# Performance work log

Hardware: AMD Instinct MI355X
Metric: run time of the kernel (lower is better)

The kernel has to match this reference:

```python
import jax, jax.numpy as jnp
import numpy as np

DIM = 1024
NUM_HEADS = 16
HEAD_DIM = DIM // NUM_HEADS
SCALE = HEAD_DIM ** (-0.5)


def setup_inputs() -> dict:
    key = jax.random.key(0)
    ks = jax.random.split(key, 10)
    b, nq, nkv = 1, 4096, 4096
    s = DIM ** -0.5
    return {
        "q": jax.random.normal(ks[0], (b, nq, DIM), jnp.float32),
        "kv": jax.random.normal(ks[1], (b, nkv, DIM), jnp.float32),
        "q_w": jax.random.normal(ks[2], (DIM, DIM), jnp.float32) * s,
        "q_b": jnp.zeros((DIM,), jnp.float32),
        "k_w": jax.random.normal(ks[3], (DIM, DIM), jnp.float32) * s,
        "k_b": jnp.zeros((DIM,), jnp.float32),
        "v_w": jax.random.normal(ks[4], (DIM, DIM), jnp.float32) * s,
        "v_b": jnp.zeros((DIM,), jnp.float32),
        "o_w": jax.random.normal(ks[5], (DIM, DIM), jnp.float32) * s,
        "o_b": jnp.zeros((DIM,), jnp.float32),
    }


def reference(q, kv, q_w, q_b, k_w, k_b, v_w, v_b, o_w, o_b):
    b, nq, _ = q.shape
    nkv = kv.shape[1]
    h, c = NUM_HEADS, HEAD_DIM
    # projections (torch Linear: x @ W^T + b); split into heads
    qh = (q @ q_w.T + q_b).reshape(b, nq, h, c).transpose(0, 2, 1, 3)   # b h nq c
    kh = (kv @ k_w.T + k_b).reshape(b, nkv, h, c).transpose(0, 2, 1, 3)  # b h nkv c
    vh = (kv @ v_w.T + v_b).reshape(b, nkv, h, c).transpose(0, 2, 1, 3)  # b h nkv c
    # full attention score matrix (non-fused, as in source)
    attn = jnp.einsum('bhqc,bhkc->bhqk', qh, kh) * SCALE
    attn = jax.nn.softmax(attn, axis=-1)
    out = jnp.einsum('bhqk,bhkc->bhqc', attn, vh)  # b h nq c
    out = out.transpose(0, 2, 1, 3).reshape(b, nq, h * c)
    out = out @ o_w.T + o_b
    return out
```

## Files before the change

kernel.cpp:

```cpp
#include <hip/hip_runtime.h>


typedef unsigned short ushort_t;
typedef unsigned short ushort4v __attribute__((ext_vector_type(4)));
typedef unsigned short ushort8 __attribute__((ext_vector_type(8)));
typedef __bf16 bf16x8 __attribute__((ext_vector_type(8)));
typedef float f32x4 __attribute__((ext_vector_type(4)));
typedef float f32x16 __attribute__((ext_vector_type(16)));
typedef unsigned int uint4v __attribute__((ext_vector_type(4)));

#define SEQ 4096
#define DIM 1024
#define NH 16
#define HD 64
#define QSCALE 0.18033688011112042f

__device__ inline ushort_t fcvt(float f) {
    return __builtin_bit_cast(ushort_t, (__bf16)f);
}
__device__ inline bf16x8 frag_of(ushort8 t) {
    return __builtin_bit_cast(bf16x8, t);
}
__device__ inline bf16x8 lds_frag(const ushort_t* p) {
    return frag_of(*(const ushort8*)p);
}
__device__ inline unsigned pk2(float a, float b) {
    return (unsigned)fcvt(a) | ((unsigned)fcvt(b) << 16);
}
__device__ inline void plswap(unsigned& a, unsigned& b) {
    asm("v_permlane32_swap_b32 %0, %1" : "+v"(a), "+v"(b));
}
__device__ inline int swz(int row, int col) {
    return row * 64 + (col ^ ((row & 7) << 3));
}
__device__ __attribute__((always_inline)) inline void gload16(
    const ushort_t* g, ushort_t* l)
{
    __builtin_amdgcn_global_load_lds(
        (const __attribute__((address_space(1))) void*)g,
        (__attribute__((address_space(3))) void*)l, 16, 0, 0);
}

__global__ __launch_bounds__(256) void cvt2(
    const float* __restrict__ s0, ushort_t* __restrict__ d0,
    const float* __restrict__ s1, ushort_t* __restrict__ d1, int n8)
{
    const float* s = blockIdx.y ? s1 : s0;
    ushort_t*    d = blockIdx.y ? d1 : d0;
    int i = blockIdx.x * 256 + threadIdx.x;
    if (i >= n8) return;
    const f32x4* sp = (const f32x4*)s + (size_t)i * 2;
    f32x4 a = sp[0], b = sp[1];
    ushort8 o;
    for (int k = 0; k < 4; ++k) { o[k] = fcvt(a[k]); o[k + 4] = fcvt(b[k]); }
    *((ushort8*)d + i) = o;
}

__global__ __launch_bounds__(256) void cvt4(
    const float* __restrict__ s0, ushort_t* __restrict__ d0,
    const float* __restrict__ s1, ushort_t* __restrict__ d1,
    const float* __restrict__ s2, ushort_t* __restrict__ d2,
    const float* __restrict__ s3, ushort_t* __restrict__ d3, int n8)
{
    const float* ss[4] = {s0, s1, s2, s3};
    ushort_t*    dd[4] = {d0, d1, d2, d3};
    const float* s = ss[blockIdx.y];
    ushort_t*    d = dd[blockIdx.y];
    int i = blockIdx.x * 256 + threadIdx.x;
    if (i >= n8) return;
    const f32x4* sp = (const f32x4*)s + (size_t)i * 2;
    f32x4 a = sp[0], b = sp[1];
    ushort8 o;
    for (int k = 0; k < 4; ++k) { o[k] = fcvt(a[k]); o[k + 4] = fcvt(b[k]); }
    *((ushort8*)d + i) = o;
}

template<int BN>
__device__ __attribute__((always_inline)) inline void gemm_core2(
    const ushort_t* __restrict__ A, const ushort_t* __restrict__ W,
    int m0, int n0, int tid, f32x4 (&acc)[4][BN / 32], ushort_t* sLDS)
{
    constexpr int TA = 128 * 64;
    constexpr int TB = BN * 64;
    ushort_t* const aB0 = sLDS;
    ushort_t* const aB1 = sLDS + TA;
    ushort_t* const bB0 = sLDS + 2 * TA;
    ushort_t* const bB1 = sLDS + 2 * TA + TB;

    const int w    = tid >> 6;
    const int lane = tid & 63;
    const int quad = lane >> 4;
    const int l15  = lane & 15;
    const int wm   = w >> 1;
    const int wn   = w & 1;

    const int srow = lane >> 3;
    const int sch  = ((lane & 7) ^ srow) << 3;
    const ushort_t* Ag = A + (size_t)(m0 + w * 32 + srow) * DIM + sch;
    const ushort_t* Bg = W + (size_t)(n0 + w * (BN / 4) + srow) * DIM + sch;
    const int aOff = w * 2048;
    const int bOff = w * (BN * 16);

    for (int i = 0; i < 4; ++i)
        gload16(Ag + (size_t)(i * 8) * DIM, aB0 + aOff + i * 512);
    for (int i = 0; i < BN / 32; ++i)
        gload16(Bg + (size_t)(i * 8) * DIM, bB0 + bOff + i * 512);
    __syncthreads();

    const int cxor = l15 & 7;
    for (int it = 0; it < DIM / 64; ++it) {
        const int cur = it & 1;
        ushort_t* aC = cur ? aB1 : aB0;
        ushort_t* bC = cur ? bB1 : bB0;
        ushort_t* aN = cur ? aB0 : aB1;
        ushort_t* bN = cur ? bB0 : bB1;

        if (it + 1 < DIM / 64) {
            const int k0 = (it + 1) * 64;
            for (int i = 0; i < 4; ++i)
                gload16(Ag + k0 + (size_t)(i * 8) * DIM, aN + aOff + i * 512);
            for (int i = 0; i < BN / 32; ++i)
                gload16(Bg + k0 + (size_t)(i * 8) * DIM, bN + bOff + i * 512);
        }

        for (int kk = 0; kk < 2; ++kk) {
            const int cq = kk * 4 + quad;
            bf16x8 af[4], bf[BN / 32];
            for (int i = 0; i < 4; ++i) {
                int row = wm * 64 + i * 16 + l15;
                af[i] = lds_frag(aC + row * 64 + ((cq ^ cxor) << 3));
            }
            for (int j = 0; j < BN / 32; ++j) {
                int row = wn * (BN / 2) + j * 16 + l15;
                bf[j] = lds_frag(bC + row * 64 + ((cq ^ cxor) << 3));
            }
            for (int i = 0; i < 4; ++i)
                for (int j = 0; j < BN / 32; ++j)
                    acc[i][j] = __builtin_amdgcn_mfma_f32_16x16x32_bf16(
                        af[i], bf[j], acc[i][j], 0, 0, 0);
        }
        __syncthreads();
    }
}

__global__ __launch_bounds__(256, 2) void proj3(
    const ushort_t* __restrict__ Qb, const ushort_t* __restrict__ KVb,
    const ushort_t* __restrict__ qwb, const ushort_t* __restrict__ kwb,
    const ushort_t* __restrict__ vwb,
    const float* __restrict__ q_b, const float* __restrict__ k_b,
    const float* __restrict__ v_b,
    ushort_t* __restrict__ Qp, ushort_t* __restrict__ Kp,
    ushort_t* __restrict__ VpT)
{
    __shared__ __align__(1024) ushort_t sLDS[32768];

    const int z = blockIdx.z;
    const ushort_t* A = z ? KVb : Qb;
    const ushort_t* W = (z == 0) ? qwb : (z == 1 ? kwb : vwb);
    const float* bias = (z == 0) ? q_b : (z == 1 ? k_b : v_b);
    const int tid = threadIdx.x;
    const int m0 = blockIdx.y * 128;
    const int n0 = blockIdx.x * 128;

    f32x4 acc[4][4] = {};
    gemm_core2<128>(A, W, m0, n0, tid, acc, sLDS);

    const int lane = tid & 63, quad = lane >> 4, l15 = lane & 15;
    const int wm = (tid >> 6) >> 1, wn = (tid >> 6) & 1;

    if (z == 2) {
        const int TSTR = 136;
        for (int j = 0; j < 4; ++j) {
            int col = wn * 64 + j * 16 + l15;
            float bj = bias[n0 + col];
            for (int i = 0; i < 4; ++i) {
                int row = wm * 64 + i * 16 + quad * 4;
                ushort4v o4;
                for (int r = 0; r < 4; ++r) o4[r] = fcvt(acc[i][j][r] + bj);
                *(ushort4v*)(sLDS + col * TSTR + row) = o4;
            }
        }
        __syncthreads();
        const int vrow = tid >> 1;
        const int vc   = (tid & 1) * 64;
        ushort_t* dst = VpT + (size_t)(n0 + vrow) * SEQ + m0 + vc;
        const ushort_t* src = sLDS + vrow * TSTR + vc;
        for (int k = 0; k < 8; ++k)
            *(ushort8*)(dst + k * 8) = *(const ushort8*)(src + k * 8);
    } else {
        const float scale = (z == 0) ? QSCALE : 1.0f;
        ushort_t* C = z ? Kp : Qp;
        for (int j = 0; j < 4; ++j) {
            int col = n0 + wn * 64 + j * 16 + l15;
            float bj = bias[col];
            for (int i = 0; i < 4; ++i) {
                int row = m0 + wm * 64 + i * 16 + quad * 4;
                for (int r = 0; r < 4; ++r)
                    C[(size_t)(row + r) * DIM + col] =
                        fcvt((acc[i][j][r] + bj) * scale);
            }
        }
    }
}

__global__ __launch_bounds__(256, 2) void gemm_out(
    const ushort_t* __restrict__ A, const ushort_t* __restrict__ W,
    const float* __restrict__ bias, float* __restrict__ C)
{
    __shared__ __align__(1024) ushort_t sLDS[24576];

    const int tid = threadIdx.x;
    const int m0 = blockIdx.y * 128;
    const int n0 = blockIdx.x * 64;

    f32x4 acc[4][2] = {};
    gemm_core2<64>(A, W, m0, n0, tid, acc, sLDS);

    const int lane = tid & 63, quad = lane >> 4, l15 = lane & 15;
    const int wm = (tid >> 6) >> 1, wn = (tid >> 6) & 1;
    for (int j = 0; j < 2; ++j) {
        int col = n0 + wn * 32 + j * 16 + l15;
        float bj = bias[col];
        for (int i = 0; i < 4; ++i) {
            int row = m0 + wm * 64 + i * 16 + quad * 4;
            for (int r = 0; r < 4; ++r)
                C[(size_t)(row + r) * DIM + col] = acc[i][j][r] + bj;
        }
    }
}

#define TILE 4096
#define BUFE (2 * TILE)
__global__ __launch_bounds__(256, 2) void attn_kernel(
    const ushort_t* __restrict__ Q, const ushort_t* __restrict__ K,
    const ushort_t* __restrict__ VT, ushort_t* __restrict__ O)
{
    __shared__ __align__(16) ushort_t sB[2 * BUFE];

    const int tid  = threadIdx.x;
    const int w    = tid >> 6;
    const int lane = tid & 63;
    const int l31  = lane & 31;
    const int hi   = lane >> 5;
    const int h    = blockIdx.x;
    const int q0   = blockIdx.y * 128 + w * 32;
    const int hHD  = h * HD;

    const int srow0 = tid >> 3;
    const int srow1 = srow0 + 32;
    const int sch   = (tid & 7) << 3;
    const ushort_t* Kg0 = K  + (size_t)srow0 * DIM + hHD + sch;
    const ushort_t* Kg1 = K  + (size_t)srow1 * DIM + hHD + sch;
    const ushort_t* Vg0 = VT + (size_t)(hHD + srow0) * SEQ + sch;
    const ushort_t* Vg1 = VT + (size_t)(hHD + srow1) * SEQ + sch;
    const int lk0 = swz(srow0, sch), lk1 = swz(srow1, sch);

    const ushort_t* qb = Q + (size_t)(q0 + l31) * DIM + hHD + hi * 8;
    bf16x8 qf[4];
    for (int ks = 0; ks < 4; ++ks)
        qf[ks] = frag_of(*(const ushort8*)(qb + ks * 16));

    *(ushort8*)(sB + lk0)        = *(const ushort8*)(Kg0);
    *(ushort8*)(sB + lk1)        = *(const ushort8*)(Kg1);
    *(ushort8*)(sB + TILE + lk0) = *(const ushort8*)(Vg0);
    *(ushort8*)(sB + TILE + lk1) = *(const ushort8*)(Vg1);
    __syncthreads();

    f32x16 oacc[2] = {};
    float l_i = 0.f;

    for (int it = 0; it < SEQ / 64; ++it) {
        const int cur = it & 1;
        const int kvn = (it + 1) * 64;
        ushort_t* bK = sB + cur * BUFE;
        ushort_t* bV = bK + TILE;

        ushort8 gk0, gk1, gv0, gv1;
        if (kvn < SEQ) {
            gk0 = *(const ushort8*)(Kg0 + (size_t)kvn * DIM);
            gk1 = *(const ushort8*)(Kg1 + (size_t)kvn * DIM);
            gv0 = *(const ushort8*)(Vg0 + kvn);
            gv1 = *(const ushort8*)(Vg1 + kvn);
        }

        bf16x8 kf[8], vf[8];
        for (int t = 0; t < 2; ++t)
            for (int ks = 0; ks < 4; ++ks) {
                int r = t * 32 + l31;
                kf[t * 4 + ks] = lds_frag(bK + swz(r, ks * 16 + hi * 8));
            }
        for (int dt = 0; dt < 2; ++dt)
            for (int ks = 0; ks < 4; ++ks) {
                int r = dt * 32 + l31;
                vf[ks * 2 + dt] = lds_frag(bV + swz(r, ks * 16 + hi * 8));
            }

        f32x16 sacc[2] = {};
        for (int t = 0; t < 2; ++t)
            for (int ks = 0; ks < 4; ++ks)
                sacc[t] = __builtin_amdgcn_mfma_f32_32x32x16_bf16(
                    kf[t * 4 + ks], qf[ks], sacc[t], 0, 0, 0);

        float lp = 0.f;
        for (int t = 0; t < 2; ++t)
            for (int r = 0; r < 16; ++r) {
                float p = __builtin_amdgcn_exp2f(sacc[t][r]);
                sacc[t][r] = p;
                lp += p;
            }
        l_i += lp + __shfl_xor(lp, 32);

        for (int ks = 0; ks < 4; ++ks) {
            const int t = ks >> 1, s8 = (ks & 1) * 8;
            unsigned p00 = pk2(sacc[t][s8 + 0], sacc[t][s8 + 1]);
            unsigned p01 = pk2(sacc[t][s8 + 2], sacc[t][s8 + 3]);
            unsigned p10 = pk2(sacc[t][s8 + 4], sacc[t][s8 + 5]);
            unsigned p11 = pk2(sacc[t][s8 + 6], sacc[t][s8 + 7]);
            plswap(p00, p10);
            plswap(p01, p11);
            uint4v wv; wv[0] = p00; wv[1] = p01; wv[2] = p10; wv[3] = p11;
            bf16x8 pf = __builtin_bit_cast(bf16x8, wv);
            for (int dt = 0; dt < 2; ++dt)
                oacc[dt] = __builtin_amdgcn_mfma_f32_32x32x16_bf16(
                    vf[ks * 2 + dt], pf, oacc[dt], 0, 0, 0);
        }

        if (kvn < SEQ) {
            ushort_t* nB = sB + (cur ^ 1) * BUFE;
            *(ushort8*)(nB + lk0)        = gk0;
            *(ushort8*)(nB + lk1)        = gk1;
            *(ushort8*)(nB + TILE + lk0) = gv0;
            *(ushort8*)(nB + TILE + lk1) = gv1;
        }
        __syncthreads();
    }

    float inv = 1.f / l_i;
    int qrow = q0 + l31;
    for (int dt = 0; dt < 2; ++dt)
        for (int g = 0; g < 4; ++g) {
            ushort4v o4;
            for (int r = 0; r < 4; ++r) o4[r] = fcvt(oacc[dt][g * 4 + r] * inv);
            *(ushort4v*)(O + (size_t)qrow * DIM + hHD + dt * 32 + g * 8 + hi * 4) = o4;
        }
}

extern "C" void kernel_launch(void* const* d_in, const int* in_sizes, int n_in,
                              void* d_out, int out_size, void* d_ws, size_t ws_size,
                              hipStream_t stream)
{
    const float* q   = (const float*)d_in[0];
    const float* kv  = (const float*)d_in[1];
    const float* q_w = (const float*)d_in[2];
    const float* q_b = (const float*)d_in[3];
    const float* k_w = (const float*)d_in[4];
    const float* k_b = (const float*)d_in[5];
    const float* v_w = (const float*)d_in[6];
    const float* v_b = (const float*)d_in[7];
    const float* o_w = (const float*)d_in[8];
    const float* o_b = (const float*)d_in[9];
    float* out = (float*)d_out;

    const size_t SD = (size_t)SEQ * DIM;
    const size_t WW = (size_t)DIM * DIM;
    ushort_t* Qp  = (ushort_t*)d_ws;
    ushort_t* Kp  = Qp + SD;
    ushort_t* VpT = Kp + SD;
    ushort_t* AO  = VpT + SD;
    ushort_t* Qb  = AO;
    ushort_t* KVb = AO + SD;
    ushort_t* qwb = KVb + SD;
    ushort_t* kwb = qwb + WW;
    ushort_t* vwb = kwb + WW;
    ushort_t* owb = vwb + WW;

    cvt2<<<dim3((unsigned)(SD / 8 / 256), 2), 256, 0, stream>>>(
        q, Qb, kv, KVb, (int)(SD / 8));
    cvt4<<<dim3((unsigned)(WW / 8 / 256), 4), 256, 0, stream>>>(
        q_w, qwb, k_w, kwb, v_w, vwb, o_w, owb, (int)(WW / 8));

    proj3<<<dim3(DIM / 128, SEQ / 128, 3), 256, 0, stream>>>(
        Qb, KVb, qwb, kwb, vwb, q_b, k_b, v_b, Qp, Kp, VpT);
    attn_kernel<<<dim3(NH, SEQ / 128), 256, 0, stream>>>(Qp, Kp, VpT, AO);
    gemm_out<<<dim3(DIM / 64, SEQ / 128), 256, 0, stream>>>(AO, owb, o_b, out);
}
```

Before: 245.3 us.

## Shrink GEMM K-tile to 32 with new swizzle, smaller out tiles, MFMA row sums

The GEMM core now stages 32-wide K slices instead of 64, using a new LDS swizzle, which cuts shared memory per block so proj3 and gemm_out can run at higher occupancy (launch bounds 3 and 4). gemm_out drops to 64x64 tiles, doubling its grid. In attention, the softmax denominator is accumulated with an extra MFMA against a ones vector instead of scalar adds plus a cross-lane shuffle. The trade-offs are twice as many K iterations and barriers in the GEMMs, and an extra matrix op per attention step.

```diff
diff --git a/kernel.cpp b/kernel.cpp
--- a/kernel.cpp
+++ b/kernel.cpp
@@ -75,13 +75,13 @@
     *((ushort8*)d + i) = o;
 }
 
-template<int BN>
-__device__ __attribute__((always_inline)) inline void gemm_core2(
+template<int BM, int BN>
+__device__ __attribute__((always_inline)) inline void gemm_core3(
     const ushort_t* __restrict__ A, const ushort_t* __restrict__ W,
-    int m0, int n0, int tid, f32x4 (&acc)[4][BN / 32], ushort_t* sLDS)
-{
-    constexpr int TA = 128 * 64;
-    constexpr int TB = BN * 64;
+    int m0, int n0, int tid, f32x4 (&acc)[BM / 32][BN / 32], ushort_t* sLDS)
+{
+    constexpr int TA = BM * 32;
+    constexpr int TB = BN * 32;
     ushort_t* const aB0 = sLDS;
     ushort_t* const aB1 = sLDS + TA;
     ushort_t* const bB0 = sLDS + 2 * TA;
@@ -94,56 +94,53 @@
     const int wm   = w >> 1;
     const int wn   = w & 1;
 
-    const int srow = lane >> 3;
-    const int sch  = ((lane & 7) ^ srow) << 3;
-    const ushort_t* Ag = A + (size_t)(m0 + w * 32 + srow) * DIM + sch;
+    const int srow = lane >> 2;
+    const int sch  = (((lane & 3) ^ ((lane >> 3) & 3)) << 3);
+    const ushort_t* Ag = A + (size_t)(m0 + w * (BM / 4) + srow) * DIM + sch;
     const ushort_t* Bg = W + (size_t)(n0 + w * (BN / 4) + srow) * DIM + sch;
-    const int aOff = w * 2048;
-    const int bOff = w * (BN * 16);
-
-    for (int i = 0; i < 4; ++i)
-        gload16(Ag + (size_t)(i * 8) * DIM, aB0 + aOff + i * 512);
-    for (int i = 0; i < BN / 32; ++i)
-        gload16(Bg + (size_t)(i * 8) * DIM, bB0 + bOff + i * 512);
+    const int aOff = w * (BM / 4) * 32;
+    const int bOff = w * (BN / 4) * 32;
+
+    for (int i = 0; i < BM / 64; ++i)
+        gload16(Ag + (size_t)(i * 16) * DIM, aB0 + aOff + i * 512);
+    for (int i = 0; i < BN / 64; ++i)
+        gload16(Bg + (size_t)(i * 16) * DIM, bB0 + bOff + i * 512);
     __syncthreads();
 
-    const int cxor = l15 & 7;
-    for (int it = 0; it < DIM / 64; ++it) {
+    const int slot = (quad ^ ((l15 >> 1) & 3)) << 3;
+    for (int it = 0; it < DIM / 32; ++it) {
         const int cur = it & 1;
         ushort_t* aC = cur ? aB1 : aB0;
         ushort_t* bC = cur ? bB1 : bB0;
         ushort_t* aN = cur ? aB0 : aB1;
         ushort_t* bN = cur ? bB0 : bB1;
 
-        if (it + 1 < DIM / 64) {
-            const int k0 = (it + 1) * 64;
-            for (int i = 0; i < 4; ++i)
-                gload16(Ag + k0 + (size_t)(i * 8) * DIM, aN + aOff + i * 512);
-            for (int i = 0; i < BN / 32; ++i)
-                gload16(Bg + k0 + (size_t)(i * 8) * DIM, bN + bOff + i * 512);
-        }
-
-        for (int kk = 0; kk < 2; ++kk) {
-            const int cq = kk * 4 + quad;
-            bf16x8 af[4], bf[BN / 32];
-            for (int i = 0; i < 4; ++i) {
-                int row = wm * 64 + i * 16 + l15;
-                af[i] = lds_frag(aC + row * 64 + ((cq ^ cxor) << 3));
-            }
-            for (int j = 0; j < BN / 32; ++j) {
-                int row = wn * (BN / 2) + j * 16 + l15;
-                bf[j] = lds_frag(bC + row * 64 + ((cq ^ cxor) << 3));
-            }
-            for (int i = 0; i < 4; ++i)
-                for (int j = 0; j < BN / 32; ++j)
-                    acc[i][j] = __builtin_amdgcn_mfma_f32_16x16x32_bf16(
-                        af[i], bf[j], acc[i][j], 0, 0, 0);
-        }
+        if (it + 1 < DIM / 32) {
+            const int k0 = (it + 1) * 32;
+            for (int i = 0; i < BM / 64; ++i)
+                gload16(Ag + k0 + (size_t)(i * 16) * DIM, aN + aOff + i * 512);
+            for (int i = 0; i < BN / 64; ++i)
+                gload16(Bg + k0 + (size_t)(i * 16) * DIM, bN + bOff + i * 512);
+        }
+
+        bf16x8 af[BM / 32], bf[BN / 32];
+        for (int i = 0; i < BM / 32; ++i) {
+            int row = wm * (BM / 2) + i * 16 + l15;
+            af[i] = lds_frag(aC + row * 32 + slot);
+        }
+        for (int j = 0; j < BN / 32; ++j) {
+            int row = wn * (BN / 2) + j * 16 + l15;
+            bf[j] = lds_frag(bC + row * 32 + slot);
+        }
+        for (int i = 0; i < BM / 32; ++i)
+            for (int j = 0; j < BN / 32; ++j)
+                acc[i][j] = __builtin_amdgcn_mfma_f32_16x16x32_bf16(
+                    af[i], bf[j], acc[i][j], 0, 0, 0);
         __syncthreads();
     }
 }
 
-__global__ __launch_bounds__(256, 2) void proj3(
+__global__ __launch_bounds__(256, 3) void proj3(
     const ushort_t* __restrict__ Qb, const ushort_t* __restrict__ KVb,
     const ushort_t* __restrict__ qwb, const ushort_t* __restrict__ kwb,
     const ushort_t* __restrict__ vwb,
@@ -152,7 +149,7 @@
     ushort_t* __restrict__ Qp, ushort_t* __restrict__ Kp,
     ushort_t* __restrict__ VpT)
 {
-    __shared__ __align__(1024) ushort_t sLDS[32768];
+    __shared__ __align__(1024) ushort_t sLDS[17536];
 
     const int z = blockIdx.z;
     const ushort_t* A = z ? KVb : Qb;
@@ -163,7 +160,7 @@
     const int n0 = blockIdx.x * 128;
 
     f32x4 acc[4][4] = {};
-    gemm_core2<128>(A, W, m0, n0, tid, acc, sLDS);
+    gemm_core3<128, 128>(A, W, m0, n0, tid, acc, sLDS);
 
     const int lane = tid & 63, quad = lane >> 4, l15 = lane & 15;
     const int wm = (tid >> 6) >> 1, wn = (tid >> 6) & 1;
@@ -203,26 +200,26 @@
     }
 }
 
-__global__ __launch_bounds__(256, 2) void gemm_out(
+__global__ __launch_bounds__(256, 4) void gemm_out(
     const ushort_t* __restrict__ A, const ushort_t* __restrict__ W,
     const float* __restrict__ bias, float* __restrict__ C)
 {
-    __shared__ __align__(1024) ushort_t sLDS[24576];
+    __shared__ __align__(1024) ushort_t sLDS[8192];
 
     const int tid = threadIdx.x;
-    const int m0 = blockIdx.y * 128;
+    const int m0 = blockIdx.y * 64;
     const int n0 = blockIdx.x * 64;
 
-    f32x4 acc[4][2] = {};
-    gemm_core2<64>(A, W, m0, n0, tid, acc, sLDS);
+    f32x4 acc[2][2] = {};
+    gemm_core3<64, 64>(A, W, m0, n0, tid, acc, sLDS);
 
     const int lane = tid & 63, quad = lane >> 4, l15 = lane & 15;
     const int wm = (tid >> 6) >> 1, wn = (tid >> 6) & 1;
     for (int j = 0; j < 2; ++j) {
         int col = n0 + wn * 32 + j * 16 + l15;
         float bj = bias[col];
-        for (int i = 0; i < 4; ++i) {
-            int row = m0 + wm * 64 + i * 16 + quad * 4;
+        for (int i = 0; i < 2; ++i) {
+            int row = m0 + wm * 32 + i * 16 + quad * 4;
             for (int r = 0; r < 4; ++r)
                 C[(size_t)(row + r) * DIM + col] = acc[i][j][r] + bj;
         }
@@ -260,6 +257,9 @@
     for (int ks = 0; ks < 4; ++ks)
         qf[ks] = frag_of(*(const ushort8*)(qb + ks * 16));
 
+    bf16x8 onef;
+    for (int i = 0; i < 8; ++i) onef[i] = (__bf16)1.0f;
+
     *(ushort8*)(sB + lk0)        = *(const ushort8*)(Kg0);
     *(ushort8*)(sB + lk1)        = *(const ushort8*)(Kg1);
     *(ushort8*)(sB + TILE + lk0) = *(const ushort8*)(Vg0);
@@ -267,7 +267,7 @@
     __syncthreads();
 
     f32x16 oacc[2] = {};
-    float l_i = 0.f;
+    f32x16 lacc = {};
 
     for (int it = 0; it < SEQ / 64; ++it) {
         const int cur = it & 1;
@@ -301,14 +301,9 @@
                 sacc[t] = __builtin_amdgcn_mfma_f32_32x32x16_bf16(
                     kf[t * 4 + ks], qf[ks], sacc[t], 0, 0, 0);
 
-        float lp = 0.f;
         for (int t = 0; t < 2; ++t)
-            for (int r = 0; r < 16; ++r) {
-                float p = __builtin_amdgcn_exp2f(sacc[t][r]);
-                sacc[t][r] = p;
-                lp += p;
-            }
-        l_i += lp + __shfl_xor(lp, 32);
+            for (int r = 0; r < 16; ++r)
+                sacc[t][r] = __builtin_amdgcn_exp2f(sacc[t][r]);
 
         for (int ks = 0; ks < 4; ++ks) {
             const int t = ks >> 1, s8 = (ks & 1) * 8;
@@ -323,6 +318,8 @@
             for (int dt = 0; dt < 2; ++dt)
                 oacc[dt] = __builtin_amdgcn_mfma_f32_32x32x16_bf16(
                     vf[ks * 2 + dt], pf, oacc[dt], 0, 0, 0);
+            lacc = __builtin_amdgcn_mfma_f32_32x32x16_bf16(
+                onef, pf, lacc, 0, 0, 0);
         }
 
         if (kvn < SEQ) {
@@ -335,7 +332,7 @@
         __syncthreads();
     }
 
-    float inv = 1.f / l_i;
+    float inv = 1.f / lacc[0];
     int qrow = q0 + l31;
     for (int dt = 0; dt < 2; ++dt)
         for (int g = 0; g < 4; ++g) {
@@ -382,5 +379,5 @@
     proj3<<<dim3(DIM / 128, SEQ / 128, 3), 256, 0, stream>>>(
         Qb, KVb, qwb, kwb, vwb, q_b, k_b, v_b, Qp, Kp, VpT);
     attn_kernel<<<dim3(NH, SEQ / 128), 256, 0, stream>>>(Qp, Kp, VpT, AO);
-    gemm_out<<<dim3(DIM / 64, SEQ / 128), 256, 0, stream>>>(AO, owb, o_b, out);
-}
+    gemm_out<<<dim3(DIM / 64, SEQ / 64), 256, 0, stream>>>(AO, owb, o_b, out);
+}
```

After: 247.0 us. No clear change (+0.7%).
